# Kernel optimization log

Hardware: AMD Instinct MI355X
Metric: run time of the kernel (lower is better)

The kernel has to match this reference:

```python
import jax, jax.numpy as jnp
import numpy as np

N_SEND = 12288   # 12 * 32^2
N_REC = 49152    # 12 * 64^2
E = 196608       # 4 * N_REC (knn with k=4)
D = 256
EIN, EOUT = 4, 256
LIN_IN, LIN_OUT = 512, 256
B = 2


def setup_inputs() -> dict:
    key = jax.random.key(0)
    ks = jax.random.split(key, 12)
    s = 0.05
    x = jax.random.normal(ks[0], (B, N_SEND, D), jnp.float32)
    edge_attr = jax.random.normal(ks[1], (E, EIN), jnp.float32)
    idx_send = jax.random.randint(ks[2], (E,), 0, N_SEND, dtype=jnp.int32)
    idx_rec = jnp.sort(jax.random.randint(ks[3], (E,), 0, N_REC, dtype=jnp.int32))
    return {
        "x": x,
        "edge_attr": edge_attr,
        "idx_send": idx_send,
        "idx_rec": idx_rec,
        "We1": jax.random.normal(ks[4], (EIN, EOUT), jnp.float32) * s,
        "be1": jnp.zeros((EOUT,), jnp.float32),
        "We2": jax.random.normal(ks[5], (EOUT, EOUT), jnp.float32) * s,
        "be2": jnp.zeros((EOUT,), jnp.float32),
        "Wl1": jax.random.normal(ks[6], (LIN_IN, LIN_OUT), jnp.float32) * s,
        "bl1": jnp.zeros((LIN_OUT,), jnp.float32),
        "Wl2": jax.random.normal(ks[7], (LIN_OUT, LIN_OUT), jnp.float32) * s,
        "bl2": jnp.zeros((LIN_OUT,), jnp.float32),
    }


def reference(x, edge_attr, idx_send, idx_rec, We1, be1, We2, be2, Wl1, bl1, Wl2, bl2):
    # edge embedder MLP: Linear -> GELU -> Linear   [E, EOUT]
    ef = jax.nn.gelu(edge_attr @ We1 + be1) @ We2 + be2
    # gather sender node features by edge           [B, E, D]
    v_s = x[:, idx_send, :]
    # concat gathered features with (batch-broadcast) edge embeddings [B, E, D+EOUT]
    ef_b = jnp.broadcast_to(ef[None], (v_s.shape[0],) + ef.shape)
    v_s_prime = jnp.concatenate([v_s, ef_b], axis=-1)
    # scatter_sum over receiver index along edge dim -> [B, N_REC, LIN_IN]
    agg = jax.vmap(lambda m: jax.ops.segment_sum(m, idx_rec, num_segments=N_REC))(v_s_prime)
    # final FeedForward: Linear -> GELU -> Linear
    return jax.nn.gelu(agg @ Wl1 + bl1) @ Wl2 + bl2
```

## Files before the change

kernel.cpp:

```cpp
#include <hip/hip_runtime.h>
#include <hip/hip_bf16.h>

#define N_SEND 12288
#define N_REC  49152
#define NEDGE  196608
#define AREC   16
#define AECAP  256

typedef __attribute__((ext_vector_type(8)))  short short8;
typedef __attribute__((ext_vector_type(4)))  short shortx4;
typedef __attribute__((ext_vector_type(4)))  float floatx4;
typedef __attribute__((ext_vector_type(16))) float floatx16;
typedef __attribute__((ext_vector_type(4)))  unsigned int uintx4;

__device__ inline short f2bs(float f) {
    __hip_bfloat16 h = __float2bfloat16(f);
    return *reinterpret_cast<short*>(&h);
}
__device__ inline float gelu_tanh(float x) {
    const float k0 = 0.7978845608028654f;
    float u = k0 * (x + 0.044715f * x * x * x);
    float e = __expf(2.0f * u);
    float t = 1.0f - 2.0f / (e + 1.0f);
    return 0.5f * x * (1.0f + t);
}

__device__ inline void gload_lds16(const short* g, short* l) {
    __builtin_amdgcn_global_load_lds(
        (const __attribute__((address_space(1))) unsigned int*)g,
        (__attribute__((address_space(3))) unsigned int*)l, 16, 0, 0);
}

__global__ void prep_kernel(const float* __restrict__ We2, const float* __restrict__ be2,
                            const float* __restrict__ Wl1, const float* __restrict__ Wl2,
                            short* __restrict__ BT1, short* __restrict__ WT2,
                            float* __restrict__ cvec) {
    int i = blockIdx.x;
    int n = threadIdx.x;
    if (i < 256) {
        float acc = 0.f;
        for (int j = 0; j < 256; ++j)
            acc += We2[i * 256 + j] * Wl1[(256 + j) * 256 + n];
        BT1[n * 512 + i]       = f2bs(Wl1[i * 256 + n]);
        BT1[n * 512 + 256 + i] = f2bs(acc);
        WT2[n * 256 + i]       = f2bs(Wl2[i * 256 + n]);
    } else {
        float acc = 0.f;
        for (int j = 0; j < 256; ++j)
            acc += be2[j] * Wl1[(256 + j) * 256 + n];
        cvec[n] = acc;
    }
}

__global__ void xcast_kernel(const float* __restrict__ X, short* __restrict__ Xb) {
    int i = (blockIdx.x * 256 + threadIdx.x) * 8;
    floatx4 v0 = *(const floatx4*)(X + i);
    floatx4 v1 = *(const floatx4*)(X + i + 4);
    short8 p;
#pragma unroll
    for (int j = 0; j < 4; ++j) { p[j] = f2bs(v0[j]); p[j + 4] = f2bs(v1[j]); }
    *(short8*)(Xb + i) = p;
}

__global__ void bounds_kernel(const int* __restrict__ idx_rec, int* __restrict__ bnd) {
    int r = blockIdx.x * 256 + threadIdx.x;
    if (r > N_REC) return;
    int lo = 0, hi = NEDGE;
    while (lo < hi) { int mid = (lo + hi) >> 1; if (idx_rec[mid] < r) lo = mid + 1; else hi = mid; }
    bnd[r] = lo;
}

__global__ __launch_bounds__(512, 6)
void aggregate(const int* __restrict__ idx_send, const int* __restrict__ bnd,
               const float* __restrict__ EA, const float* __restrict__ We1,
               const float* __restrict__ be1, const short* __restrict__ Xb,
               short* __restrict__ AGX, short* __restrict__ AGH) {
    __shared__ __attribute__((aligned(16))) short XTs[32 * 32 * 8];
    __shared__ __attribute__((aligned(16))) short HTs[32 * 16 * 8];
    __shared__ int   sb[AREC + 1];
    __shared__ int   s_idx[AECAP];
    __shared__ __attribute__((aligned(16))) float s_ea[AECAP * 4];

    int t = threadIdx.x;
    int r0 = blockIdx.x * AREC;
    if (t <= AREC) sb[t] = bnd[r0 + t];
    __syncthreads();
    int e0 = sb[0], eN = sb[AREC];

    int cg = t & 31;
    int b  = (t >> 5) & 1;
    int rh = t >> 6;
    int c8 = cg * 8;
    int hc = c8 + 4 * b;

    floatx4 w0 = *(const floatx4*)(We1 + hc);
    floatx4 w1 = *(const floatx4*)(We1 + 256 + hc);
    floatx4 w2 = *(const floatx4*)(We1 + 512 + hc);
    floatx4 w3 = *(const floatx4*)(We1 + 768 + hc);
    floatx4 bb = *(const floatx4*)(be1 + hc);
    const short* xb_t = Xb + (size_t)b * N_SEND * 256 + c8;

    float xacc[2][8];
    float hacc[2][4];
#pragma unroll
    for (int r = 0; r < 2; ++r) {
#pragma unroll
        for (int c = 0; c < 8; ++c) xacc[r][c] = 0.f;
#pragma unroll
        for (int c = 0; c < 4; ++c) hacc[r][c] = 0.f;
    }

    for (int base = e0; base < eN; base += AECAP) {
        int cnt = min(AECAP, eN - base);
        __syncthreads();
        for (int i = t; i < cnt; i += 512) {
            s_idx[i] = idx_send[base + i];
            *(floatx4*)(s_ea + 4 * i) = *(const floatx4*)(EA + (size_t)(base + i) * 4);
        }
        __syncthreads();
#pragma unroll
        for (int r = 0; r < 2; ++r) {
            int rl = rh * 2 + r;
            int es = max(sb[rl], base);
            int ee = min(sb[rl + 1], base + cnt);
            for (int e = es; e < ee; ++e) {
                int li = e - base;
                int s = s_idx[li];
                uintx4 xv = *(const uintx4*)(xb_t + (size_t)s * 256);
                floatx4 a = *(const floatx4*)(s_ea + 4 * li);
#pragma unroll
                for (int dw = 0; dw < 4; ++dw) {
                    xacc[r][2 * dw]     += __builtin_bit_cast(float, xv[dw] << 16);
                    xacc[r][2 * dw + 1] += __builtin_bit_cast(float, xv[dw] & 0xffff0000u);
                }
#pragma unroll
                for (int j = 0; j < 4; ++j) {
                    float u = a[0] * w0[j] + a[1] * w1[j] + a[2] * w2[j] + a[3] * w3[j] + bb[j];
                    hacc[r][j] += gelu_tanh(u);
                }
            }
        }
    }
#pragma unroll
    for (int r = 0; r < 2; ++r) {
        int rl = rh * 2 + r;
        short8 xp;
#pragma unroll
        for (int c = 0; c < 8; ++c) xp[c] = f2bs(xacc[r][c]);
        *(short8*)(XTs + (cg * 32 + b * 16 + rl) * 8) = xp;
        shortx4 hp;
#pragma unroll
        for (int c = 0; c < 4; ++c) hp[c] = f2bs(hacc[r][c]);
        *(shortx4*)(HTs + (cg * 16 + rl) * 8 + 4 * b) = hp;
    }
    __syncthreads();
    {
        const uintx4* xs = (const uintx4*)XTs;
        uintx4* xd = (uintx4*)(AGX + (size_t)blockIdx.x * (32 * 32 * 8));
        xd[t]       = xs[t];
        xd[t + 512] = xs[t + 512];
        const uintx4* hs = (const uintx4*)HTs;
        uintx4* hd = (uintx4*)(AGH + (size_t)blockIdx.x * (32 * 16 * 8));
        hd[t] = hs[t];
    }
}

__global__ __launch_bounds__(512, 2)
void gemm(const int* __restrict__ bnd, const short* __restrict__ AGX,
          const short* __restrict__ AGH, const short* __restrict__ BT1,
          const short* __restrict__ WT2, const float* __restrict__ cvec,
          const float* __restrict__ bl1, const float* __restrict__ bl2,
          float* __restrict__ OUT) {
    __shared__ __attribute__((aligned(16))) short XT[4 * 32 * 32 * 8];
    __shared__ __attribute__((aligned(16))) short HT[4 * 32 * 16 * 8];
    __shared__ int sb[65];

    int t = threadIdx.x;
    int blk = blockIdx.x;
    int r0 = blk * 64;
    if (t < 65) sb[t] = bnd[r0 + t];

    {
        const short* sx = AGX + (size_t)blk * (4 * 32 * 32 * 8);
        const short* sh = AGH + (size_t)blk * (4 * 32 * 16 * 8);
#pragma unroll
        for (int k = 0; k < 8; ++k) {
            int c = t + k * 512;
            gload_lds16(sx + c * 8, XT + c * 8);
        }
#pragma unroll
        for (int k = 0; k < 4; ++k) {
            int c = t + k * 512;
            gload_lds16(sh + c * 8, HT + c * 8);
        }
    }
    __syncthreads();

    int w = t >> 6, lane = t & 63;
    int m = lane & 31, q = lane >> 5;
    int wcol = w * 32;
    floatx16 acc[4];
#pragma unroll
    for (int i = 0; i < 4; ++i)
#pragma unroll
        for (int j = 0; j < 16; ++j) acc[i][j] = 0.f;

    const short* Bp1 = BT1 + (size_t)(wcol + m) * 512 + q * 8;
    short8 bfA[4], bfB[4];
#pragma unroll
    for (int kk = 0; kk < 4; ++kk) bfA[kk] = *(const short8*)(Bp1 + kk * 16);

#pragma unroll
    for (int ci = 0; ci < 8; ++ci) {
        int kc = ci * 64;
        const short8* bc = (ci & 1) ? bfB : bfA;
        short8*       bn = (ci & 1) ? bfA : bfB;
        if (ci < 7) {
#pragma unroll
            for (int kk = 0; kk < 4; ++kk)
                bn[kk] = *(const short8*)(Bp1 + kc + 64 + kk * 16);
        }
#pragma unroll
        for (int kk = 0; kk < 4; ++kk) {
            int f = (kc >> 3) + 2 * kk + q;
#pragma unroll
            for (int rt = 0; rt < 4; ++rt) {
                const short* ap = (ci < 4)
                    ? (XT + rt * 8192 + f * 256 + m * 8)
                    : (HT + rt * 4096 + (f - 32) * 128 + (m & 15) * 8);
                short8 a = *(const short8*)ap;
                acc[rt] = __builtin_amdgcn_mfma_f32_32x32x16_bf16(bc[kk], a, acc[rt], 0, 0, 0);
            }
        }
    }
    __syncthreads();

#pragma unroll
    for (int rt = 0; rt < 4; ++rt) {
        int row = rt * 32 + m;
        int rl = rt * 16 + (m & 15);
        float cntv = (float)(sb[rl + 1] - sb[rl]);
#pragma unroll
        for (int qd = 0; qd < 4; ++qd) {
            int c0 = wcol + qd * 8 + q * 4;
            floatx4 cv  = *(const floatx4*)(cvec + c0);
            floatx4 b1v = *(const floatx4*)(bl1 + c0);
            shortx4 pk;
#pragma unroll
            for (int j = 0; j < 4; ++j)
                pk[j] = f2bs(gelu_tanh(acc[rt][qd * 4 + j] + cntv * cv[j] + b1v[j]));
            *(shortx4*)(XT + ((w * 4 + qd) * 128 + row) * 8 + q * 4) = pk;
        }
#pragma unroll
        for (int j = 0; j < 16; ++j) acc[rt][j] = 0.f;
    }
    __syncthreads();

    const short* Bp2 = WT2 + (size_t)(wcol + m) * 256 + q * 8;
#pragma unroll
    for (int kk = 0; kk < 4; ++kk) bfA[kk] = *(const short8*)(Bp2 + kk * 16);

#pragma unroll
    for (int ci = 0; ci < 4; ++ci) {
        int kc = ci * 64;
        const short8* bc = (ci & 1) ? bfB : bfA;
        short8*       bn = (ci & 1) ? bfA : bfB;
        if (ci < 3) {
#pragma unroll
            for (int kk = 0; kk < 4; ++kk)
                bn[kk] = *(const short8*)(Bp2 + kc + 64 + kk * 16);
        }
#pragma unroll
        for (int kk = 0; kk < 4; ++kk) {
            int f2 = (kc >> 3) + 2 * kk + q;
#pragma unroll
            for (int rt = 0; rt < 4; ++rt) {
                short8 a = *(const short8*)(XT + (f2 * 128 + rt * 32 + m) * 8);
                acc[rt] = __builtin_amdgcn_mfma_f32_32x32x16_bf16(bc[kk], a, acc[rt], 0, 0, 0);
            }
        }
    }

#pragma unroll
    for (int rt = 0; rt < 4; ++rt) {
        int batch = (m >> 4) & 1;
        int rl = rt * 16 + (m & 15);
        size_t obase = ((size_t)batch * N_REC + r0 + rl) * 256;
#pragma unroll
        for (int qd = 0; qd < 4; ++qd) {
            int c0 = wcol + qd * 8 + q * 4;
            floatx4 bv = *(const floatx4*)(bl2 + c0);
            floatx4 o;
#pragma unroll
            for (int j = 0; j < 4; ++j)
                o[j] = acc[rt][qd * 4 + j] + bv[j];
            *(floatx4*)(OUT + obase + c0) = o;
        }
    }
}

extern "C" void kernel_launch(void* const* d_in, const int* in_sizes, int n_in,
                              void* d_out, int out_size, void* d_ws, size_t ws_size,
                              hipStream_t stream) {
    const float* x        = (const float*)d_in[0];
    const float* ea       = (const float*)d_in[1];
    const int*   idx_send = (const int*)d_in[2];
    const int*   idx_rec  = (const int*)d_in[3];
    const float* We1      = (const float*)d_in[4];
    const float* be1      = (const float*)d_in[5];
    const float* We2      = (const float*)d_in[6];
    const float* be2      = (const float*)d_in[7];
    const float* Wl1      = (const float*)d_in[8];
    const float* bl1      = (const float*)d_in[9];
    const float* Wl2      = (const float*)d_in[10];
    const float* bl2      = (const float*)d_in[11];
    float* out = (float*)d_out;
    char*  ws  = (char*)d_ws;

    short* BT1  = (short*)(ws + 0);
    short* WT2  = (short*)(ws + 262144);
    float* cvec = (float*)(ws + 393216);
    int*   bnd  = (int*)  (ws + 397312);
    short* Xb   = (short*)(ws + 1048576);
    short* AGX  = (short*)(ws + 13631488);
    short* AGH  = (short*)(ws + 63963136);

    prep_kernel<<<257, 256, 0, stream>>>(We2, be2, Wl1, Wl2, BT1, WT2, cvec);
    xcast_kernel<<<(2 * N_SEND * 256) / (256 * 8), 256, 0, stream>>>(x, Xb);
    bounds_kernel<<<(N_REC + 1 + 255) / 256, 256, 0, stream>>>(idx_rec, bnd);
    aggregate<<<N_REC / AREC, 512, 0, stream>>>(idx_send, bnd, ea, We1, be1, Xb, AGX, AGH);
    gemm<<<N_REC / 64, 512, 0, stream>>>(bnd, AGX, AGH, BT1, WT2, cvec, bl1, bl2, out);
}
```

Before: 297.4 us.

## Interleave bf16 node features by batch and shrink gemm tile to 32 receivers

The cast kernel now stores both batch copies of each sender node next to each other (node-major, batch-interleaved), so the gather in aggregate reads one contiguous 1KB row per sender instead of two far-apart rows. The gemm kernel processes 32 receivers per block with two accumulators instead of 64 with four, halves its LDS footprint and raises occupancy to 4 blocks per CU. It also drops the B-fragment double buffering, loading weights inline. In the gemm, the edge-embedding (H) operand is shared across both batch halves. The trade-off is more blocks re-reading the weight matrices and less software prefetch of B fragments.

```diff
diff --git a/kernel.cpp b/kernel.cpp
--- a/kernel.cpp
+++ b/kernel.cpp
@@ -6,6 +6,7 @@
 #define NEDGE  196608
 #define AREC   16
 #define AECAP  256
+#define GREC   32
 
 typedef __attribute__((ext_vector_type(8)))  short short8;
 typedef __attribute__((ext_vector_type(4)))  short shortx4;
@@ -54,12 +55,16 @@
 
 __global__ void xcast_kernel(const float* __restrict__ X, short* __restrict__ Xb) {
     int i = (blockIdx.x * 256 + threadIdx.x) * 8;
+    int row = i >> 8;
+    int c   = i & 255;
+    int bb_ = (row >= N_SEND) ? 1 : 0;
+    int n   = row - bb_ * N_SEND;
     floatx4 v0 = *(const floatx4*)(X + i);
     floatx4 v1 = *(const floatx4*)(X + i + 4);
     short8 p;
 #pragma unroll
     for (int j = 0; j < 4; ++j) { p[j] = f2bs(v0[j]); p[j + 4] = f2bs(v1[j]); }
-    *(short8*)(Xb + i) = p;
+    *(short8*)(Xb + (size_t)n * 512 + bb_ * 256 + c) = p;
 }
 
 __global__ void bounds_kernel(const int* __restrict__ idx_rec, int* __restrict__ bnd) {
@@ -98,7 +103,7 @@
     floatx4 w2 = *(const floatx4*)(We1 + 512 + hc);
     floatx4 w3 = *(const floatx4*)(We1 + 768 + hc);
     floatx4 bb = *(const floatx4*)(be1 + hc);
-    const short* xb_t = Xb + (size_t)b * N_SEND * 256 + c8;
+    const short* xb_t = Xb + b * 256 + c8;
 
     float xacc[2][8];
     float hacc[2][4];
@@ -126,7 +131,7 @@
             for (int e = es; e < ee; ++e) {
                 int li = e - base;
                 int s = s_idx[li];
-                uintx4 xv = *(const uintx4*)(xb_t + (size_t)s * 256);
+                uintx4 xv = *(const uintx4*)(xb_t + (size_t)s * 512);
                 floatx4 a = *(const floatx4*)(s_ea + 4 * li);
 #pragma unroll
                 for (int dw = 0; dw < 4; ++dw) {
@@ -165,33 +170,33 @@
     }
 }
 
-__global__ __launch_bounds__(512, 2)
+__global__ __launch_bounds__(512, 4)
 void gemm(const int* __restrict__ bnd, const short* __restrict__ AGX,
           const short* __restrict__ AGH, const short* __restrict__ BT1,
           const short* __restrict__ WT2, const float* __restrict__ cvec,
           const float* __restrict__ bl1, const float* __restrict__ bl2,
           float* __restrict__ OUT) {
-    __shared__ __attribute__((aligned(16))) short XT[4 * 32 * 32 * 8];
-    __shared__ __attribute__((aligned(16))) short HT[4 * 32 * 16 * 8];
-    __shared__ int sb[65];
+    __shared__ __attribute__((aligned(16))) short XTL[16384];
+    __shared__ __attribute__((aligned(16))) short HTL[8192];
+    __shared__ int sb[GREC + 1];
 
     int t = threadIdx.x;
     int blk = blockIdx.x;
-    int r0 = blk * 64;
-    if (t < 65) sb[t] = bnd[r0 + t];
+    int r0 = blk * GREC;
+    if (t <= GREC) sb[t] = bnd[r0 + t];
 
     {
-        const short* sx = AGX + (size_t)blk * (4 * 32 * 32 * 8);
-        const short* sh = AGH + (size_t)blk * (4 * 32 * 16 * 8);
-#pragma unroll
-        for (int k = 0; k < 8; ++k) {
-            int c = t + k * 512;
-            gload_lds16(sx + c * 8, XT + c * 8);
-        }
+        const short* sx = AGX + (size_t)blk * 16384;
+        const short* sh = AGH + (size_t)blk * 8192;
 #pragma unroll
         for (int k = 0; k < 4; ++k) {
             int c = t + k * 512;
-            gload_lds16(sh + c * 8, HT + c * 8);
+            gload_lds16(sx + c * 8, XTL + c * 8);
+        }
+#pragma unroll
+        for (int k = 0; k < 2; ++k) {
+            int c = t + k * 512;
+            gload_lds16(sh + c * 8, HTL + c * 8);
         }
     }
     __syncthreads();
@@ -199,93 +204,72 @@
     int w = t >> 6, lane = t & 63;
     int m = lane & 31, q = lane >> 5;
     int wcol = w * 32;
-    floatx16 acc[4];
-#pragma unroll
-    for (int i = 0; i < 4; ++i)
-#pragma unroll
-        for (int j = 0; j < 16; ++j) acc[i][j] = 0.f;
+    int a2 = m >> 4, rl = m & 15;
+    floatx16 acc0, acc1;
+#pragma unroll
+    for (int j = 0; j < 16; ++j) { acc0[j] = 0.f; acc1[j] = 0.f; }
 
     const short* Bp1 = BT1 + (size_t)(wcol + m) * 512 + q * 8;
-    short8 bfA[4], bfB[4];
-#pragma unroll
-    for (int kk = 0; kk < 4; ++kk) bfA[kk] = *(const short8*)(Bp1 + kk * 16);
-
 #pragma unroll
     for (int ci = 0; ci < 8; ++ci) {
-        int kc = ci * 64;
-        const short8* bc = (ci & 1) ? bfB : bfA;
-        short8*       bn = (ci & 1) ? bfA : bfB;
-        if (ci < 7) {
-#pragma unroll
-            for (int kk = 0; kk < 4; ++kk)
-                bn[kk] = *(const short8*)(Bp1 + kc + 64 + kk * 16);
-        }
 #pragma unroll
         for (int kk = 0; kk < 4; ++kk) {
-            int f = (kc >> 3) + 2 * kk + q;
-#pragma unroll
-            for (int rt = 0; rt < 4; ++rt) {
-                const short* ap = (ci < 4)
-                    ? (XT + rt * 8192 + f * 256 + m * 8)
-                    : (HT + rt * 4096 + (f - 32) * 128 + (m & 15) * 8);
-                short8 a = *(const short8*)ap;
-                acc[rt] = __builtin_amdgcn_mfma_f32_32x32x16_bf16(bc[kk], a, acc[rt], 0, 0, 0);
+            short8 bv = *(const short8*)(Bp1 + ci * 64 + kk * 16);
+            int f = ci * 8 + 2 * kk + q;
+            short8 a0, a1;
+            if (ci < 4) {
+                const short* px = XTL + a2 * 8192 + (f * 32 + rl) * 8;
+                a0 = *(const short8*)px;
+                a1 = *(const short8*)(px + 128);
+            } else {
+                short8 h = *(const short8*)(HTL + a2 * 4096 + ((f - 32) * 16 + rl) * 8);
+                a0 = h; a1 = h;
             }
-        }
-    }
-    __syncthreads();
-
-#pragma unroll
-    for (int rt = 0; rt < 4; ++rt) {
-        int row = rt * 32 + m;
-        int rl = rt * 16 + (m & 15);
-        float cntv = (float)(sb[rl + 1] - sb[rl]);
+            acc0 = __builtin_amdgcn_mfma_f32_32x32x16_bf16(bv, a0, acc0, 0, 0, 0);
+            acc1 = __builtin_amdgcn_mfma_f32_32x32x16_bf16(bv, a1, acc1, 0, 0, 0);
+        }
+    }
+    __syncthreads();
+
+    {
+        float cntv = (float)(sb[m + 1] - sb[m]);
 #pragma unroll
         for (int qd = 0; qd < 4; ++qd) {
             int c0 = wcol + qd * 8 + q * 4;
             floatx4 cv  = *(const floatx4*)(cvec + c0);
             floatx4 b1v = *(const floatx4*)(bl1 + c0);
-            shortx4 pk;
-#pragma unroll
-            for (int j = 0; j < 4; ++j)
-                pk[j] = f2bs(gelu_tanh(acc[rt][qd * 4 + j] + cntv * cv[j] + b1v[j]));
-            *(shortx4*)(XT + ((w * 4 + qd) * 128 + row) * 8 + q * 4) = pk;
-        }
-#pragma unroll
-        for (int j = 0; j < 16; ++j) acc[rt][j] = 0.f;
+            shortx4 p0, p1;
+#pragma unroll
+            for (int j = 0; j < 4; ++j) {
+                p0[j] = f2bs(gelu_tanh(acc0[qd * 4 + j] + cntv * cv[j] + b1v[j]));
+                p1[j] = f2bs(gelu_tanh(acc1[qd * 4 + j] + cntv * cv[j] + b1v[j]));
+            }
+            *(shortx4*)(XTL + ((w * 4 + qd) * 64 + m) * 8 + q * 4)      = p0;
+            *(shortx4*)(XTL + ((w * 4 + qd) * 64 + 32 + m) * 8 + q * 4) = p1;
+        }
+#pragma unroll
+        for (int j = 0; j < 16; ++j) { acc0[j] = 0.f; acc1[j] = 0.f; }
     }
     __syncthreads();
 
     const short* Bp2 = WT2 + (size_t)(wcol + m) * 256 + q * 8;
 #pragma unroll
-    for (int kk = 0; kk < 4; ++kk) bfA[kk] = *(const short8*)(Bp2 + kk * 16);
-
-#pragma unroll
     for (int ci = 0; ci < 4; ++ci) {
-        int kc = ci * 64;
-        const short8* bc = (ci & 1) ? bfB : bfA;
-        short8*       bn = (ci & 1) ? bfA : bfB;
-        if (ci < 3) {
-#pragma unroll
-            for (int kk = 0; kk < 4; ++kk)
-                bn[kk] = *(const short8*)(Bp2 + kc + 64 + kk * 16);
-        }
 #pragma unroll
         for (int kk = 0; kk < 4; ++kk) {
-            int f2 = (kc >> 3) + 2 * kk + q;
-#pragma unroll
-            for (int rt = 0; rt < 4; ++rt) {
-                short8 a = *(const short8*)(XT + (f2 * 128 + rt * 32 + m) * 8);
-                acc[rt] = __builtin_amdgcn_mfma_f32_32x32x16_bf16(bc[kk], a, acc[rt], 0, 0, 0);
-            }
-        }
-    }
-
-#pragma unroll
-    for (int rt = 0; rt < 4; ++rt) {
-        int batch = (m >> 4) & 1;
-        int rl = rt * 16 + (m & 15);
-        size_t obase = ((size_t)batch * N_REC + r0 + rl) * 256;
+            short8 bv = *(const short8*)(Bp2 + ci * 64 + kk * 16);
+            int f2 = ci * 8 + 2 * kk + q;
+            short8 a0 = *(const short8*)(XTL + (f2 * 64 + m) * 8);
+            short8 a1 = *(const short8*)(XTL + (f2 * 64 + 32 + m) * 8);
+            acc0 = __builtin_amdgcn_mfma_f32_32x32x16_bf16(bv, a0, acc0, 0, 0, 0);
+            acc1 = __builtin_amdgcn_mfma_f32_32x32x16_bf16(bv, a1, acc1, 0, 0, 0);
+        }
+    }
+
+#pragma unroll
+    for (int rt = 0; rt < 2; ++rt) {
+        const floatx16& ac = rt ? acc1 : acc0;
+        size_t obase = ((size_t)rt * N_REC + r0 + m) * 256;
 #pragma unroll
         for (int qd = 0; qd < 4; ++qd) {
             int c0 = wcol + qd * 8 + q * 4;
@@ -293,7 +277,7 @@
             floatx4 o;
 #pragma unroll
             for (int j = 0; j < 4; ++j)
-                o[j] = acc[rt][qd * 4 + j] + bv[j];
+                o[j] = ac[qd * 4 + j] + bv[j];
             *(floatx4*)(OUT + obase + c0) = o;
         }
     }
@@ -329,5 +313,5 @@
     xcast_kernel<<<(2 * N_SEND * 256) / (256 * 8), 256, 0, stream>>>(x, Xb);
     bounds_kernel<<<(N_REC + 1 + 255) / 256, 256, 0, stream>>>(idx_rec, bnd);
     aggregate<<<N_REC / AREC, 512, 0, stream>>>(idx_send, bnd, ea, We1, be1, Xb, AGX, AGH);
-    gemm<<<N_REC / 64, 512, 0, stream>>>(bnd, AGX, AGH, BT1, WT2, cvec, bl1, bl2, out);
-}
+    gemm<<<N_REC / GREC, 512, 0, stream>>>(bnd, AGX, AGH, BT1, WT2, cvec, bl1, bl2, out);
+}
```

New measurement: 301.9 us. Within noise of the previous version (+1.5%).
